# Kernel tuning notes

Hardware: AMD Instinct MI355X
Metric: run time of the kernel (lower is better)

## Reference

```python
import jax, jax.numpy as jnp
import numpy as np

B, G = 2, 8192
IMG_H, IMG_W = 256, 256
CHUNK = 64  # gaussians composited per scan step


def setup_inputs() -> dict:
    key = jax.random.key(0)
    ks = jax.random.split(key, 7)
    # means inside the image
    means2d = jax.random.uniform(ks[0], (B, G, 2), dtype=jnp.float32) * jnp.array([IMG_W, IMG_H], jnp.float32)
    # positive-definite conic (inverse 2D covariance): a, b, c with a,c>0 and b^2 < a*c
    a = jax.random.uniform(ks[1], (B, G), jnp.float32, 0.02, 0.25)
    c = jax.random.uniform(ks[2], (B, G), jnp.float32, 0.02, 0.25)
    b = (jax.random.uniform(ks[3], (B, G), jnp.float32) * 2.0 - 1.0) * 0.5 * jnp.sqrt(a * c)
    conics = jnp.stack([a, b, c], axis=-1)
    colors = jax.random.uniform(ks[4], (B, G, 3), dtype=jnp.float32)
    opacities = jax.random.uniform(ks[5], (B, G), jnp.float32, 0.05, 1.0)
    depths = jax.random.uniform(ks[6], (B, G), jnp.float32, 0.1, 10.0)
    return {"means2d": means2d, "conics": conics, "colors": colors,
            "opacities": opacities, "depths": depths,
            "image_height": IMG_H, "image_width": IMG_W}


def _rasterize(means2d, conics, colors, opacities, order, Hh, Ww):
    """Front-to-back alpha compositing of depth-ordered 2D Gaussians.

    Mathematically identical to the tile-binned/per-tile-sorted kernel: the
    tiling is only a scheduling decomposition of global depth-ordered
    over-compositing.
    """
    Bb, Gg = opacities.shape
    P = Hh * Ww
    # gather in front-to-back depth order
    gm = jnp.take_along_axis(means2d, order[..., None], axis=1)   # [B,G,2]
    gc = jnp.take_along_axis(conics, order[..., None], axis=1)    # [B,G,3]
    gl = jnp.take_along_axis(colors, order[..., None], axis=1)    # [B,G,3]
    go = jnp.take_along_axis(opacities, order, axis=1)            # [B,G]

    ys = jnp.arange(Hh, dtype=jnp.float32) + 0.5
    xs = jnp.arange(Ww, dtype=jnp.float32) + 0.5
    gy, gx = jnp.meshgrid(ys, xs, indexing='ij')
    pxf = gx.reshape(-1)  # [P]
    pyf = gy.reshape(-1)  # [P]

    n_chunks = Gg // CHUNK
    gm = gm.reshape(Bb, n_chunks, CHUNK, 2).transpose(1, 0, 2, 3)
    gc = gc.reshape(Bb, n_chunks, CHUNK, 3).transpose(1, 0, 2, 3)
    gl = gl.reshape(Bb, n_chunks, CHUNK, 3).transpose(1, 0, 2, 3)
    go = go.reshape(Bb, n_chunks, CHUNK).transpose(1, 0, 2)

    def step(carry, ch):
        img, T = carry                      # [B,P,3], [B,P] transmittance
        m, cn, cl, op = ch
        dx = pxf[None, None, :] - m[..., 0:1]   # [B,C,P]
        dy = pyf[None, None, :] - m[..., 1:2]
        a = cn[..., 0:1]
        b = cn[..., 1:2]
        c = cn[..., 2:3]
        power = -0.5 * (a * dx * dx + c * dy * dy) - b * dx * dy
        alpha = op[..., None] * jnp.exp(jnp.minimum(power, 0.0))
        alpha = jnp.minimum(alpha, 0.999)
        alpha = jnp.where(alpha < 1.0 / 255.0, 0.0, alpha)      # kernel skip-threshold
        Tc = jnp.cumprod(1.0 - alpha, axis=1)                   # within-chunk transmittance
        Tb = T[:, None, :] * jnp.concatenate(
            [jnp.ones_like(Tc[:, :1]), Tc[:, :-1]], axis=1)     # exclusive product
        img = img + jnp.einsum('bcp,bcd->bpd', Tb * alpha, cl)
        T = T * Tc[:, -1, :]
        return (img, T), None

    init = (jnp.zeros((Bb, P, 3), jnp.float32), jnp.ones((Bb, P), jnp.float32))
    (img, T), _ = jax.lax.scan(step, init, (gm, gc, gl, go))
    return img.reshape(Bb, Hh, Ww, 3), (1.0 - T).reshape(Bb, Hh, Ww)


def reference(means2d, conics, colors, opacities, depths, image_height, image_width):
    order = jnp.argsort(depths, axis=1)  # front-to-back
    image, alpha = _rasterize(means2d, conics, colors, opacities, order,
                              int(image_height), int(image_width))
    return image, alpha
```

## Files before the change

kernel.cpp:

```cpp
#include <hip/hip_runtime.h>
#include <stdint.h>

#define GCOUNT 8192
#define BATCH 2
#define IMGH 256
#define IMGW 256
#define TILE 16
#define TILES_X (IMGW / TILE)
#define TILES_Y (IMGH / TILE)
#define MAXLIST 1024

#define LDS_BAR() do { asm volatile("s_waitcnt lgkmcnt(0)" ::: "memory"); \
                       __builtin_amdgcn_s_barrier(); } while (0)

__global__ __launch_bounds__(256) void prep(
    const float* __restrict__ means, const float* __restrict__ conics,
    const float* __restrict__ colors, const float* __restrict__ opac,
    const float* __restrict__ depths,
    float4* __restrict__ gdat,
    float* __restrict__ gblue,
    uint32_t* __restrict__ gbbox,
    unsigned long long* __restrict__ gkey)
{
    const int t = blockIdx.x * 256 + threadIdx.x;
    if (t >= BATCH * GCOUNT) return;
    const int g = t & (GCOUNT - 1);

    const float mx  = means[t * 2 + 0];
    const float my  = means[t * 2 + 1];
    const float ca  = conics[t * 3 + 0];
    const float cb  = conics[t * 3 + 1];
    const float cc  = conics[t * 3 + 2];
    const float cr  = colors[t * 3 + 0];
    const float cg  = colors[t * 3 + 1];
    const float cbl = colors[t * 3 + 2];
    const float op  = opac[t];
    const float dep = depths[t];

    const float tt  = __logf(255.0f * op);
    const float det = ca * cc - cb * cb;
    const float inv = 2.0f * tt / det;
    const float dxm = sqrtf(inv * cc) + 1.0f;
    const float dym = sqrtf(inv * ca) + 1.0f;

    int x0 = max(0, (int)floorf((mx - dxm) * (1.0f / TILE)));
    int x1 = min(TILES_X - 1, (int)floorf((mx + dxm) * (1.0f / TILE)));
    int y0 = max(0, (int)floorf((my - dym) * (1.0f / TILE)));
    int y1 = min(TILES_Y - 1, (int)floorf((my + dym) * (1.0f / TILE)));
    uint32_t bb;
    if (x1 < x0 || y1 < y0)
        bb = 0xFFu;
    else
        bb = (uint32_t)x0 | ((uint32_t)x1 << 8) |
             ((uint32_t)y0 << 16) | ((uint32_t)y1 << 24);

    gdat[t * 2 + 0] = make_float4(mx, my, -0.5f * ca, -cb);
    gdat[t * 2 + 1] = make_float4(-0.5f * cc, op, cr, cg);
    gblue[t] = cbl;
    gbbox[t] = bb;
    gkey[t]  = ((unsigned long long)__float_as_uint(dep) << 13) | (unsigned)g;
}

__global__ __launch_bounds__(1024, 8) void raster(
    const float4* __restrict__ gdat, const float* __restrict__ gblue,
    const uint32_t* __restrict__ gbbox, const unsigned long long* __restrict__ gkey,
    float* __restrict__ out)
{
    __shared__ unsigned long long keys[MAXLIST];
    __shared__ float4 sdat[MAXLIST][2];
    __shared__ float  sblue[MAXLIST];
    __shared__ uint16_t sinv[MAXLIST];
    __shared__ float4 xch[7][256];
    __shared__ int    scnt;

    const int tid  = threadIdx.x;
    const int lane = tid & 63;
    const int wid  = tid >> 6;
    const int tx = blockIdx.x, ty = blockIdx.y, b = blockIdx.z;
    const int bg = b * GCOUNT;

    if (tid == 0) scnt = 0;
    LDS_BAR();

    const unsigned long long mlt = (1ull << lane) - 1ull;
    {
        uint32_t v[8];
#pragma unroll
        for (int k = 0; k < 8; ++k)
            v[k] = gbbox[bg + k * 1024 + tid];
        bool hit[8];
        unsigned long long bal[8];
        int cnts[8], sum = 0;
#pragma unroll
        for (int k = 0; k < 8; ++k) {
            const int x0 = v[k] & 0xFF, x1 = (v[k] >> 8) & 0xFF;
            const int y0 = (v[k] >> 16) & 0xFF, y1 = (v[k] >> 24) & 0xFF;
            hit[k] = (tx >= x0) & (tx <= x1) & (ty >= y0) & (ty <= y1);
            bal[k] = __ballot(hit[k]);
            cnts[k] = __popcll(bal[k]);
            sum += cnts[k];
        }
        int wbase = 0;
        if (lane == 0 && sum) wbase = atomicAdd(&scnt, sum);
        wbase = __shfl(wbase, 0);
#pragma unroll
        for (int k = 0; k < 8; ++k) {
            if (hit[k]) {
                const int pos = wbase + __popcll(bal[k] & mlt);
                if (pos < MAXLIST)
                    keys[pos] = (gkey[bg + k * 1024 + tid] << 10) | (unsigned)pos;
            }
            wbase += cnts[k];
        }
    }
    LDS_BAR();
    const int cnt = min(scnt, MAXLIST);

    const bool h0 = tid < cnt;
    float4 r0a, r0b;
    float r0c = 0.f;
    if (h0) {
        const int g0 = (int)((keys[tid] >> 10) & 8191);
        r0a = gdat[(bg + g0) * 2 + 0];
        r0b = gdat[(bg + g0) * 2 + 1];
        r0c = gblue[bg + g0];
    }

    int P = 64;
    while (P < cnt) P <<= 1;
    for (int i = cnt + tid; i < P; i += 1024) keys[i] = ~0ull;
    LDS_BAR();

    if ((wid << 6) < P) {
        unsigned long long key = keys[(wid << 6) | lane];
        const bool descBlock = (wid & 1);
#pragma unroll
        for (int k = 2; k <= 64; k <<= 1) {
            for (int j = k >> 1; j > 0; j >>= 1) {
                const unsigned long long other = __shfl_xor(key, j);
                const bool asc   = (((lane & k) == 0) != descBlock);
                const bool lower = ((lane & j) == 0);
                const unsigned long long mn = (key < other) ? key : other;
                const unsigned long long mx = (key < other) ? other : key;
                key = (asc == lower) ? mn : mx;
            }
        }
        keys[(wid << 6) | lane] = key;
    }
    LDS_BAR();

    for (int k = 128; k <= P; k <<= 1) {
        for (int j = k >> 1; j >= 64; j >>= 1) {
            const int i = tid;
            if (i < P) {
                const int ixj = i ^ j;
                if (ixj > i) {
                    const unsigned long long A = keys[i], Bv = keys[ixj];
                    const bool asc = ((i & k) == 0);
                    if ((A > Bv) == asc) { keys[i] = Bv; keys[ixj] = A; }
                }
            }
            LDS_BAR();
        }
        if ((wid << 6) < P) {
            const int base = wid << 6;
            unsigned long long key = keys[base | lane];
            const bool asc = ((base & k) == 0);
#pragma unroll
            for (int j = 32; j > 0; j >>= 1) {
                const unsigned long long other = __shfl_xor(key, j);
                const bool lower = ((lane & j) == 0);
                const unsigned long long mn = (key < other) ? key : other;
                const unsigned long long mx = (key < other) ? other : key;
                key = (asc == lower) ? mn : mx;
            }
            keys[base | lane] = key;
        }
        LDS_BAR();
    }

    for (int i = tid; i < cnt; i += 1024)
        sinv[(int)(keys[i] & 1023u)] = (uint16_t)i;
    LDS_BAR();
    if (h0) {
        const int q = sinv[tid];
        sdat[q][0] = r0a;
        sdat[q][1] = r0b;
        sblue[q]   = r0c;
    }
    LDS_BAR();

    const int seg = wid >> 1;
    const int grp = wid & 1;
    const int p0  = (grp << 7) | (lane << 1);
    const int px0 = tx * TILE + (p0 & 15);
    const int py  = ty * TILE + (p0 >> 4);
    const float pxf = px0 + 0.5f, pyf = py + 0.5f;
    const int lo = (cnt * seg) >> 3;
    const int hi = (cnt * (seg + 1)) >> 3;

    float T0 = 1.f, ir0 = 0.f, ig0 = 0.f, ib0 = 0.f;
    float T1 = 1.f, ir1 = 0.f, ig1 = 0.f, ib1 = 0.f;

    for (int s = lo; s < hi; ++s) {
        const float4 a0 = sdat[s][0];
        const float4 a1 = sdat[s][1];
        const float  bl = sblue[s];
        const float dx = pxf - a0.x, dy = pyf - a0.y;
        const float qbdy = a0.w * dy;
        float pw0 = a0.z * dx * dx;
        pw0 = fmaf(a1.x * dy, dy, pw0);
        pw0 = fmaf(qbdy, dx, pw0);
        float pw1 = fmaf(a0.z, fmaf(2.f, dx, 1.f), pw0 + qbdy);
        pw0 = fminf(pw0, 0.f);
        pw1 = fminf(pw1, 0.f);
        float al0 = fminf(a1.y * __expf(pw0), 0.999f);
        float al1 = fminf(a1.y * __expf(pw1), 0.999f);
        if (al0 >= (1.0f / 255.0f)) {
            const float w = T0 * al0;
            ir0 += w * a1.z; ig0 += w * a1.w; ib0 += w * bl;
            T0 -= w;
        }
        if (al1 >= (1.0f / 255.0f)) {
            const float w = T1 * al1;
            ir1 += w * a1.z; ig1 += w * a1.w; ib1 += w * bl;
            T1 -= w;
        }
        if (((s - lo) & 7) == 7 && !__any(fmaxf(T0, T1) >= 1e-4f)) break;
    }

    if (seg) {
        xch[seg - 1][p0]     = make_float4(ir0, ig0, ib0, T0);
        xch[seg - 1][p0 | 1] = make_float4(ir1, ig1, ib1, T1);
    }
    LDS_BAR();
    if (seg == 0) {
#pragma unroll
        for (int q = 0; q < 7; ++q) {
            const float4 c = xch[q][p0];
            ir0 += T0 * c.x; ig0 += T0 * c.y; ib0 += T0 * c.z; T0 *= c.w;
            const float4 d = xch[q][p0 | 1];
            ir1 += T1 * d.x; ig1 += T1 * d.y; ib1 += T1 * d.z; T1 *= d.w;
        }
        const int pix0 = (b * IMGH + py) * IMGW + px0;
        *(float2*)&out[pix0 * 3 + 0] = make_float2(ir0, ig0);
        *(float2*)&out[pix0 * 3 + 2] = make_float2(ib0, ir1);
        *(float2*)&out[pix0 * 3 + 4] = make_float2(ig1, ib1);
        *(float2*)&out[(size_t)BATCH * IMGH * IMGW * 3 + pix0] =
            make_float2(1.0f - T0, 1.0f - T1);
    }
}

extern "C" void kernel_launch(void* const* d_in, const int* in_sizes, int n_in,
                              void* d_out, int out_size, void* d_ws, size_t ws_size,
                              hipStream_t stream) {
    const float* means  = (const float*)d_in[0];
    const float* conics = (const float*)d_in[1];
    const float* colors = (const float*)d_in[2];
    const float* opac   = (const float*)d_in[3];
    const float* depths = (const float*)d_in[4];

    char* ws = (char*)d_ws;
    const size_t NG = (size_t)BATCH * GCOUNT;
    float4*             gdat  = (float4*)ws;
    float*              gblue = (float*)(ws + NG * 32);
    uint32_t*           gbbox = (uint32_t*)(ws + NG * 36);
    unsigned long long* gkey  = (unsigned long long*)(ws + NG * 40);
    float* out = (float*)d_out;

    hipLaunchKernelGGL(prep, dim3((BATCH * GCOUNT + 255) / 256), dim3(256), 0, stream,
                       means, conics, colors, opac, depths, gdat, gblue, gbbox, gkey);
    hipLaunchKernelGGL(raster, dim3(TILES_X, TILES_Y, BATCH), dim3(1024), 0, stream,
                       gdat, gblue, gbbox, gkey, out);
}
```

Before: 32.43 us.

## Bin gaussians into per-tile lists with global atomics in prep kernel

The prep kernel now expands each gaussian's tile bounding box and appends its index to per-tile lists through global atomics. The raster kernel then reads its tile's count and list directly, so it no longer scans all 8192 bounding boxes per tile block with ballots. This removes redundant per-tile culling work. In exchange it adds a memset launch, atomic contention on popular tiles, and a gather of depth keys. List order is nondeterministic, but the later sort by depth key restores the correct order.

```diff
diff --git a/kernel.cpp b/kernel.cpp
--- a/kernel.cpp
+++ b/kernel.cpp
@@ -8,23 +8,26 @@
 #define TILE 16
 #define TILES_X (IMGW / TILE)
 #define TILES_Y (IMGH / TILE)
+#define NTILES (TILES_X * TILES_Y * BATCH)
 #define MAXLIST 1024
 
 #define LDS_BAR() do { asm volatile("s_waitcnt lgkmcnt(0)" ::: "memory"); \
                        __builtin_amdgcn_s_barrier(); } while (0)
 
-__global__ __launch_bounds__(256) void prep(
+__global__ __launch_bounds__(256) void prep_expand(
     const float* __restrict__ means, const float* __restrict__ conics,
     const float* __restrict__ colors, const float* __restrict__ opac,
     const float* __restrict__ depths,
     float4* __restrict__ gdat,
     float* __restrict__ gblue,
-    uint32_t* __restrict__ gbbox,
-    unsigned long long* __restrict__ gkey)
+    unsigned long long* __restrict__ gkey,
+    int* __restrict__ tcnt,
+    uint16_t* __restrict__ tlist)
 {
     const int t = blockIdx.x * 256 + threadIdx.x;
     if (t >= BATCH * GCOUNT) return;
     const int g = t & (GCOUNT - 1);
+    const int b = t >> 13;
 
     const float mx  = means[t * 2 + 0];
     const float my  = means[t * 2 + 1];
@@ -37,33 +40,36 @@
     const float op  = opac[t];
     const float dep = depths[t];
 
+    gdat[t * 2 + 0] = make_float4(mx, my, -0.5f * ca, -cb);
+    gdat[t * 2 + 1] = make_float4(-0.5f * cc, op, cr, cg);
+    gblue[t] = cbl;
+    gkey[t]  = ((unsigned long long)__float_as_uint(dep) << 13) | (unsigned)g;
+
     const float tt  = __logf(255.0f * op);
     const float det = ca * cc - cb * cb;
     const float inv = 2.0f * tt / det;
     const float dxm = sqrtf(inv * cc) + 1.0f;
     const float dym = sqrtf(inv * ca) + 1.0f;
 
-    int x0 = max(0, (int)floorf((mx - dxm) * (1.0f / TILE)));
-    int x1 = min(TILES_X - 1, (int)floorf((mx + dxm) * (1.0f / TILE)));
-    int y0 = max(0, (int)floorf((my - dym) * (1.0f / TILE)));
-    int y1 = min(TILES_Y - 1, (int)floorf((my + dym) * (1.0f / TILE)));
-    uint32_t bb;
-    if (x1 < x0 || y1 < y0)
-        bb = 0xFFu;
-    else
-        bb = (uint32_t)x0 | ((uint32_t)x1 << 8) |
-             ((uint32_t)y0 << 16) | ((uint32_t)y1 << 24);
-
-    gdat[t * 2 + 0] = make_float4(mx, my, -0.5f * ca, -cb);
-    gdat[t * 2 + 1] = make_float4(-0.5f * cc, op, cr, cg);
-    gblue[t] = cbl;
-    gbbox[t] = bb;
-    gkey[t]  = ((unsigned long long)__float_as_uint(dep) << 13) | (unsigned)g;
+    const int x0 = max(0, (int)floorf((mx - dxm) * (1.0f / TILE)));
+    const int x1 = min(TILES_X - 1, (int)floorf((mx + dxm) * (1.0f / TILE)));
+    const int y0 = max(0, (int)floorf((my - dym) * (1.0f / TILE)));
+    const int y1 = min(TILES_Y - 1, (int)floorf((my + dym) * (1.0f / TILE)));
+    if (x1 < x0 || y1 < y0) return;
+
+    for (int tyi = y0; tyi <= y1; ++tyi) {
+        for (int txi = x0; txi <= x1; ++txi) {
+            const int tile = (b * TILES_Y + tyi) * TILES_X + txi;
+            const int pos = atomicAdd(&tcnt[tile], 1);
+            if (pos < MAXLIST) tlist[tile * MAXLIST + pos] = (uint16_t)g;
+        }
+    }
 }
 
 __global__ __launch_bounds__(1024, 8) void raster(
     const float4* __restrict__ gdat, const float* __restrict__ gblue,
-    const uint32_t* __restrict__ gbbox, const unsigned long long* __restrict__ gkey,
+    const unsigned long long* __restrict__ gkey,
+    const int* __restrict__ tcnt, const uint16_t* __restrict__ tlist,
     float* __restrict__ out)
 {
     __shared__ unsigned long long keys[MAXLIST];
@@ -71,56 +77,22 @@
     __shared__ float  sblue[MAXLIST];
     __shared__ uint16_t sinv[MAXLIST];
     __shared__ float4 xch[7][256];
-    __shared__ int    scnt;
 
     const int tid  = threadIdx.x;
     const int lane = tid & 63;
     const int wid  = tid >> 6;
     const int tx = blockIdx.x, ty = blockIdx.y, b = blockIdx.z;
     const int bg = b * GCOUNT;
-
-    if (tid == 0) scnt = 0;
-    LDS_BAR();
-
-    const unsigned long long mlt = (1ull << lane) - 1ull;
-    {
-        uint32_t v[8];
-#pragma unroll
-        for (int k = 0; k < 8; ++k)
-            v[k] = gbbox[bg + k * 1024 + tid];
-        bool hit[8];
-        unsigned long long bal[8];
-        int cnts[8], sum = 0;
-#pragma unroll
-        for (int k = 0; k < 8; ++k) {
-            const int x0 = v[k] & 0xFF, x1 = (v[k] >> 8) & 0xFF;
-            const int y0 = (v[k] >> 16) & 0xFF, y1 = (v[k] >> 24) & 0xFF;
-            hit[k] = (tx >= x0) & (tx <= x1) & (ty >= y0) & (ty <= y1);
-            bal[k] = __ballot(hit[k]);
-            cnts[k] = __popcll(bal[k]);
-            sum += cnts[k];
-        }
-        int wbase = 0;
-        if (lane == 0 && sum) wbase = atomicAdd(&scnt, sum);
-        wbase = __shfl(wbase, 0);
-#pragma unroll
-        for (int k = 0; k < 8; ++k) {
-            if (hit[k]) {
-                const int pos = wbase + __popcll(bal[k] & mlt);
-                if (pos < MAXLIST)
-                    keys[pos] = (gkey[bg + k * 1024 + tid] << 10) | (unsigned)pos;
-            }
-            wbase += cnts[k];
-        }
-    }
-    LDS_BAR();
-    const int cnt = min(scnt, MAXLIST);
+    const int tile = (b * TILES_Y + ty) * TILES_X + tx;
+
+    const int cnt = min(tcnt[tile], MAXLIST);
 
     const bool h0 = tid < cnt;
     float4 r0a, r0b;
     float r0c = 0.f;
     if (h0) {
-        const int g0 = (int)((keys[tid] >> 10) & 8191);
+        const int g0 = tlist[tile * MAXLIST + tid];
+        keys[tid] = (gkey[bg + g0] << 10) | (unsigned)tid;
         r0a = gdat[(bg + g0) * 2 + 0];
         r0b = gdat[(bg + g0) * 2 + 1];
         r0c = gblue[bg + g0];
@@ -264,12 +236,14 @@
     const size_t NG = (size_t)BATCH * GCOUNT;
     float4*             gdat  = (float4*)ws;
     float*              gblue = (float*)(ws + NG * 32);
-    uint32_t*           gbbox = (uint32_t*)(ws + NG * 36);
-    unsigned long long* gkey  = (unsigned long long*)(ws + NG * 40);
+    unsigned long long* gkey  = (unsigned long long*)(ws + NG * 36);
+    int*                tcnt  = (int*)(ws + NG * 44);
+    uint16_t*           tlist = (uint16_t*)(ws + NG * 44 + NTILES * 4);
     float* out = (float*)d_out;
 
-    hipLaunchKernelGGL(prep, dim3((BATCH * GCOUNT + 255) / 256), dim3(256), 0, stream,
-                       means, conics, colors, opac, depths, gdat, gblue, gbbox, gkey);
+    hipMemsetAsync(tcnt, 0, NTILES * sizeof(int), stream);
+    hipLaunchKernelGGL(prep_expand, dim3((BATCH * GCOUNT + 255) / 256), dim3(256), 0, stream,
+                       means, conics, colors, opac, depths, gdat, gblue, gkey, tcnt, tlist);
     hipLaunchKernelGGL(raster, dim3(TILES_X, TILES_Y, BATCH), dim3(1024), 0, stream,
-                       gdat, gblue, gbbox, gkey, out);
+                       gdat, gblue, gkey, tcnt, tlist, out);
 }
```

New measurement: 60.05 us. 1.85x slower.

## Split gaussian list across 16 waves with 4 pixels per thread and tree merge

Applied to the files above, without the earlier changes.

The raster kernel now gives each of the 16 waves a contiguous segment of the depth-sorted list, and each thread shades 4 horizontally adjacent pixels using incremental power updates. Partial composites are then merged in a log-depth tree through LDS. Log-opacity is folded into the exponent, red and green are packed as fp16 into the second float4 so the separate blue array goes away, and the early-termination check is removed. The trade-off is reduced colour precision, more barriers in the merge, and lost early exit for saturated pixels.

```diff
diff --git a/kernel.cpp b/kernel.cpp
--- a/kernel.cpp
+++ b/kernel.cpp
@@ -1,4 +1,5 @@
 #include <hip/hip_runtime.h>
+#include <hip/hip_fp16.h>
 #include <stdint.h>
 
 #define GCOUNT 8192
@@ -18,7 +19,6 @@
     const float* __restrict__ colors, const float* __restrict__ opac,
     const float* __restrict__ depths,
     float4* __restrict__ gdat,
-    float* __restrict__ gblue,
     uint32_t* __restrict__ gbbox,
     unsigned long long* __restrict__ gkey)
 {
@@ -37,7 +37,8 @@
     const float op  = opac[t];
     const float dep = depths[t];
 
-    const float tt  = __logf(255.0f * op);
+    const float lop = __logf(op);
+    const float tt  = lop + 5.5412635f;
     const float det = ca * cc - cb * cb;
     const float inv = 2.0f * tt / det;
     const float dxm = sqrtf(inv * cc) + 1.0f;
@@ -54,24 +55,26 @@
         bb = (uint32_t)x0 | ((uint32_t)x1 << 8) |
              ((uint32_t)y0 << 16) | ((uint32_t)y1 << 24);
 
+    const __half hr = __float2half_rn(cr);
+    const __half hg = __float2half_rn(cg);
+    const uint32_t pk = ((uint32_t)__half_as_ushort(hg) << 16) |
+                        (uint32_t)__half_as_ushort(hr);
+
     gdat[t * 2 + 0] = make_float4(mx, my, -0.5f * ca, -cb);
-    gdat[t * 2 + 1] = make_float4(-0.5f * cc, op, cr, cg);
-    gblue[t] = cbl;
+    gdat[t * 2 + 1] = make_float4(-0.5f * cc, lop, __uint_as_float(pk), cbl);
     gbbox[t] = bb;
     gkey[t]  = ((unsigned long long)__float_as_uint(dep) << 13) | (unsigned)g;
 }
 
 __global__ __launch_bounds__(1024, 8) void raster(
-    const float4* __restrict__ gdat, const float* __restrict__ gblue,
-    const uint32_t* __restrict__ gbbox, const unsigned long long* __restrict__ gkey,
-    float* __restrict__ out)
+    const float4* __restrict__ gdat, const uint32_t* __restrict__ gbbox,
+    const unsigned long long* __restrict__ gkey, float* __restrict__ out)
 {
     __shared__ unsigned long long keys[MAXLIST];
     __shared__ float4 sdat[MAXLIST][2];
-    __shared__ float  sblue[MAXLIST];
     __shared__ uint16_t sinv[MAXLIST];
-    __shared__ float4 xch[7][256];
-    __shared__ int    scnt;
+    __shared__ float4 xch[8][64][4];
+    __shared__ int scnt;
 
     const int tid  = threadIdx.x;
     const int lane = tid & 63;
@@ -118,12 +121,10 @@
 
     const bool h0 = tid < cnt;
     float4 r0a, r0b;
-    float r0c = 0.f;
     if (h0) {
         const int g0 = (int)((keys[tid] >> 10) & 8191);
         r0a = gdat[(bg + g0) * 2 + 0];
         r0b = gdat[(bg + g0) * 2 + 1];
-        r0c = gblue[bg + g0];
     }
 
     int P = 64;
@@ -186,68 +187,80 @@
         const int q = sinv[tid];
         sdat[q][0] = r0a;
         sdat[q][1] = r0b;
-        sblue[q]   = r0c;
-    }
-    LDS_BAR();
-
-    const int seg = wid >> 1;
-    const int grp = wid & 1;
-    const int p0  = (grp << 7) | (lane << 1);
-    const int px0 = tx * TILE + (p0 & 15);
-    const int py  = ty * TILE + (p0 >> 4);
+    }
+    LDS_BAR();
+
+    const int px0 = tx * TILE + ((lane & 3) << 2);
+    const int py  = ty * TILE + (lane >> 2);
     const float pxf = px0 + 0.5f, pyf = py + 0.5f;
-    const int lo = (cnt * seg) >> 3;
-    const int hi = (cnt * (seg + 1)) >> 3;
-
-    float T0 = 1.f, ir0 = 0.f, ig0 = 0.f, ib0 = 0.f;
-    float T1 = 1.f, ir1 = 0.f, ig1 = 0.f, ib1 = 0.f;
+    const int lo = (cnt * wid) >> 4;
+    const int hi = (cnt * (wid + 1)) >> 4;
+
+    float T0 = 1.f, cr0 = 0.f, cg0 = 0.f, cb0 = 0.f;
+    float T1 = 1.f, cr1 = 0.f, cg1 = 0.f, cb1 = 0.f;
+    float T2 = 1.f, cr2 = 0.f, cg2 = 0.f, cb2 = 0.f;
+    float T3 = 1.f, cr3 = 0.f, cg3 = 0.f, cb3 = 0.f;
 
     for (int s = lo; s < hi; ++s) {
-        const float4 a0 = sdat[s][0];
-        const float4 a1 = sdat[s][1];
-        const float  bl = sblue[s];
-        const float dx = pxf - a0.x, dy = pyf - a0.y;
-        const float qbdy = a0.w * dy;
-        float pw0 = a0.z * dx * dx;
-        pw0 = fmaf(a1.x * dy, dy, pw0);
+        const float4 A = sdat[s][0];
+        const float4 Bv = sdat[s][1];
+        const float dx = pxf - A.x, dy = pyf - A.y;
+        const float qbdy = A.w * dy;
+        float pw0 = fmaf(A.z * dx, dx, Bv.y);
+        pw0 = fmaf(Bv.x * dy, dy, pw0);
         pw0 = fmaf(qbdy, dx, pw0);
-        float pw1 = fmaf(a0.z, fmaf(2.f, dx, 1.f), pw0 + qbdy);
-        pw0 = fminf(pw0, 0.f);
-        pw1 = fminf(pw1, 0.f);
-        float al0 = fminf(a1.y * __expf(pw0), 0.999f);
-        float al1 = fminf(a1.y * __expf(pw1), 0.999f);
-        if (al0 >= (1.0f / 255.0f)) {
-            const float w = T0 * al0;
-            ir0 += w * a1.z; ig0 += w * a1.w; ib0 += w * bl;
-            T0 -= w;
-        }
-        if (al1 >= (1.0f / 255.0f)) {
-            const float w = T1 * al1;
-            ir1 += w * a1.z; ig1 += w * a1.w; ib1 += w * bl;
-            T1 -= w;
-        }
-        if (((s - lo) & 7) == 7 && !__any(fmaxf(T0, T1) >= 1e-4f)) break;
-    }
-
-    if (seg) {
-        xch[seg - 1][p0]     = make_float4(ir0, ig0, ib0, T0);
-        xch[seg - 1][p0 | 1] = make_float4(ir1, ig1, ib1, T1);
-    }
-    LDS_BAR();
-    if (seg == 0) {
-#pragma unroll
-        for (int q = 0; q < 7; ++q) {
-            const float4 c = xch[q][p0];
-            ir0 += T0 * c.x; ig0 += T0 * c.y; ib0 += T0 * c.z; T0 *= c.w;
-            const float4 d = xch[q][p0 | 1];
-            ir1 += T1 * d.x; ig1 += T1 * d.y; ib1 += T1 * d.z; T1 *= d.w;
-        }
+        const float qa2 = A.z + A.z;
+        float stp = fmaf(qa2, dx, qbdy) + A.z;
+        const float pw1 = pw0 + stp;  stp += qa2;
+        const float pw2 = pw1 + stp;  stp += qa2;
+        const float pw3 = pw2 + stp;
+
+        const uint32_t pk = __float_as_uint(Bv.z);
+        const float gr = __half2float(__ushort_as_half((unsigned short)(pk & 0xFFFFu)));
+        const float gg = __half2float(__ushort_as_half((unsigned short)(pk >> 16)));
+        const float gb = Bv.w;
+
+        float a0 = fminf(__expf(pw0), 0.999f); a0 = (a0 < (1.f/255.f)) ? 0.f : a0;
+        float a1 = fminf(__expf(pw1), 0.999f); a1 = (a1 < (1.f/255.f)) ? 0.f : a1;
+        float a2 = fminf(__expf(pw2), 0.999f); a2 = (a2 < (1.f/255.f)) ? 0.f : a2;
+        float a3 = fminf(__expf(pw3), 0.999f); a3 = (a3 < (1.f/255.f)) ? 0.f : a3;
+
+        const float w0 = T0 * a0; cr0 = fmaf(w0, gr, cr0); cg0 = fmaf(w0, gg, cg0); cb0 = fmaf(w0, gb, cb0); T0 -= w0;
+        const float w1 = T1 * a1; cr1 = fmaf(w1, gr, cr1); cg1 = fmaf(w1, gg, cg1); cb1 = fmaf(w1, gb, cb1); T1 -= w1;
+        const float w2 = T2 * a2; cr2 = fmaf(w2, gr, cr2); cg2 = fmaf(w2, gg, cg2); cb2 = fmaf(w2, gb, cb2); T2 -= w2;
+        const float w3 = T3 * a3; cr3 = fmaf(w3, gr, cr3); cg3 = fmaf(w3, gg, cg3); cb3 = fmaf(w3, gb, cb3); T3 -= w3;
+    }
+
+    int ls = 0;
+    for (int st = 1; st < 16; st <<= 1, ++ls) {
+        const int m = (st << 1) - 1;
+        if ((wid & m) == st) {
+            const int slot = wid >> (ls + 1);
+            xch[slot][lane][0] = make_float4(cr0, cg0, cb0, T0);
+            xch[slot][lane][1] = make_float4(cr1, cg1, cb1, T1);
+            xch[slot][lane][2] = make_float4(cr2, cg2, cb2, T2);
+            xch[slot][lane][3] = make_float4(cr3, cg3, cb3, T3);
+        }
+        LDS_BAR();
+        if ((wid & m) == 0) {
+            const int slot = wid >> (ls + 1);
+            float4 e;
+            e = xch[slot][lane][0]; cr0 = fmaf(T0, e.x, cr0); cg0 = fmaf(T0, e.y, cg0); cb0 = fmaf(T0, e.z, cb0); T0 *= e.w;
+            e = xch[slot][lane][1]; cr1 = fmaf(T1, e.x, cr1); cg1 = fmaf(T1, e.y, cg1); cb1 = fmaf(T1, e.z, cb1); T1 *= e.w;
+            e = xch[slot][lane][2]; cr2 = fmaf(T2, e.x, cr2); cg2 = fmaf(T2, e.y, cg2); cb2 = fmaf(T2, e.z, cb2); T2 *= e.w;
+            e = xch[slot][lane][3]; cr3 = fmaf(T3, e.x, cr3); cg3 = fmaf(T3, e.y, cg3); cb3 = fmaf(T3, e.z, cb3); T3 *= e.w;
+        }
+        LDS_BAR();
+    }
+
+    if (wid == 0) {
         const int pix0 = (b * IMGH + py) * IMGW + px0;
-        *(float2*)&out[pix0 * 3 + 0] = make_float2(ir0, ig0);
-        *(float2*)&out[pix0 * 3 + 2] = make_float2(ib0, ir1);
-        *(float2*)&out[pix0 * 3 + 4] = make_float2(ig1, ib1);
-        *(float2*)&out[(size_t)BATCH * IMGH * IMGW * 3 + pix0] =
-            make_float2(1.0f - T0, 1.0f - T1);
+        float* o = out + (size_t)pix0 * 3;
+        *(float4*)(o + 0) = make_float4(cr0, cg0, cb0, cr1);
+        *(float4*)(o + 4) = make_float4(cg1, cb1, cr2, cg2);
+        *(float4*)(o + 8) = make_float4(cb2, cr3, cg3, cb3);
+        *(float4*)&out[(size_t)BATCH * IMGH * IMGW * 3 + pix0] =
+            make_float4(1.f - T0, 1.f - T1, 1.f - T2, 1.f - T3);
     }
 }
 
@@ -263,13 +276,12 @@
     char* ws = (char*)d_ws;
     const size_t NG = (size_t)BATCH * GCOUNT;
     float4*             gdat  = (float4*)ws;
-    float*              gblue = (float*)(ws + NG * 32);
-    uint32_t*           gbbox = (uint32_t*)(ws + NG * 36);
-    unsigned long long* gkey  = (unsigned long long*)(ws + NG * 40);
+    uint32_t*           gbbox = (uint32_t*)(ws + NG * 32);
+    unsigned long long* gkey  = (unsigned long long*)(ws + NG * 36);
     float* out = (float*)d_out;
 
     hipLaunchKernelGGL(prep, dim3((BATCH * GCOUNT + 255) / 256), dim3(256), 0, stream,
-                       means, conics, colors, opac, depths, gdat, gblue, gbbox, gkey);
+                       means, conics, colors, opac, depths, gdat, gbbox, gkey);
     hipLaunchKernelGGL(raster, dim3(TILES_X, TILES_Y, BATCH), dim3(1024), 0, stream,
-                       gdat, gblue, gbbox, gkey, out);
+                       gdat, gbbox, gkey, out);
 }
```

New measurement: 29.26 us. 9.8% less time.
